# Performance work log

Hardware: AMD Instinct MI355X
Metric: run time of the kernel (lower is better)

## Reference

```python
import jax, jax.numpy as jnp
import numpy as np

N_HEADS = 16
HEAD_SIZE = 64

def setup_inputs() -> dict:
    key = jax.random.key(0)
    k1, k2 = jax.random.split(key)
    B, N, D = 2, 2048, N_HEADS * HEAD_SIZE
    x = jax.random.normal(k1, (B, N, D), dtype=jnp.float32)
    # lecun_normal-ish scale for the QKV kernel
    W_qkv = jax.random.normal(k2, (D, 3 * D), dtype=jnp.float32) * (1.0 / np.sqrt(D))
    return {"x": x, "W_qkv": W_qkv}

def reference(x, W_qkv):
    B, N, D = x.shape
    H, Dh = N_HEADS, HEAD_SIZE
    qkv = x @ W_qkv                                  # [B,N,3D]
    q, k, v = jnp.split(qkv, 3, axis=-1)
    q = q.reshape(B, N, H, Dh)
    k = k.reshape(B, N, H, Dh)
    v = v.reshape(B, N, H, Dh)
    dist = jnp.einsum('bihd,bjhd->bhij', q, k) / jnp.sqrt(jnp.asarray(Dh, dtype=x.dtype))
    mask = jnp.tril(jnp.ones((N, N), dtype=bool))[None, None, :, :]
    dist = jnp.where(mask, dist, -jnp.inf)
    attn = jax.nn.softmax(dist, axis=-1)             # [B,H,N,N]
    out_heads = jnp.einsum('bhij,bjhd->bihd', attn, v)
    return out_heads.reshape(B, N, H * Dh)
```

## Files before the change

### kernel.cpp

```cpp
#include <hip/hip_runtime.h>

typedef __attribute__((ext_vector_type(8))) short bf16x8;
typedef __attribute__((ext_vector_type(4))) float f32x4;
typedef __attribute__((ext_vector_type(16))) float f32x16;
typedef __attribute__((ext_vector_type(2))) unsigned int u32x2;

#define DEVI static __device__ __forceinline__

namespace {
constexpr int NSEQ = 2048, NH = 16;
constexpr int D = 1024, D3 = 3072;
}

DEVI unsigned short f2bf(float f) {
  union { float f; unsigned int u; } v; v.f = f;
  unsigned int r = v.u + 0x7FFFu + ((v.u >> 16) & 1u);
  return (unsigned short)(r >> 16);
}

DEVI void gload16(const unsigned short* g, unsigned short* lds_) {
  __builtin_amdgcn_global_load_lds(
      (const __attribute__((address_space(1))) unsigned int*)g,
      (__attribute__((address_space(3))) unsigned int*)lds_, 16, 0, 0);
}

DEVI f32x4 mfma16(bf16x8 a, bf16x8 b, f32x4 c) {
  return __builtin_amdgcn_mfma_f32_16x16x32_bf16(a, b, c, 0, 0, 0);
}

DEVI f32x16 mfma32(bf16x8 a, bf16x8 b, f32x16 c) {
  return __builtin_amdgcn_mfma_f32_32x32x16_bf16(a, b, c, 0, 0, 0);
}

DEVI float exp2g(float x) {
#if __has_builtin(__builtin_amdgcn_exp2f)
  return __builtin_amdgcn_exp2f(x);
#else
  return exp2f(x);
#endif
}

DEVI unsigned int cvtpk(float a, float b) {
  unsigned int r;
  asm("v_cvt_pk_bf16_f32 %0, %1, %2" : "=v"(r) : "v"(a), "v"(b));
  return r;
}

DEVI u32x2 pswap2(unsigned int a, unsigned int b) {
  return __builtin_amdgcn_permlane32_swap(a, b, false, false);
}
DEVI float xmax_halves(float v) {
  union { float f; unsigned int u; } c; c.f = v;
  u32x2 r = pswap2(c.u, c.u);
  union { unsigned int u; float f; } x, y; x.u = r.x; y.u = r.y;
  return fmaxf(x.f, y.f);
}

union U4 { unsigned int u[4]; bf16x8 v; };

__global__ __launch_bounds__(256) void prep_k(const float* __restrict__ x,
                                              const float* __restrict__ W,
                                              unsigned short* __restrict__ xb,
                                              unsigned short* __restrict__ Wt) {
  __shared__ float t[32][33];
  const int bid = blockIdx.x;
  if (bid < 4096) {
    int i = (bid * 256 + threadIdx.x) * 4;
    float4 v = *reinterpret_cast<const float4*>(x + i);
    ushort4 o;
    o.x = f2bf(v.x); o.y = f2bf(v.y); o.z = f2bf(v.z); o.w = f2bf(v.w);
    *reinterpret_cast<ushort4*>(xb + i) = o;
  } else {
    const int b2 = bid - 4096;
    const int c0 = (b2 % 96) * 32, k0 = (b2 / 96) * 32;
    const int tx = threadIdx.x & 31, ty = threadIdx.x >> 5;
#pragma unroll
    for (int r = 0; r < 32; r += 8)
      t[ty + r][tx] = W[(size_t)(k0 + ty + r) * D3 + c0 + tx];
    __syncthreads();
#pragma unroll
    for (int r = 0; r < 32; r += 8)
      Wt[(size_t)(c0 + ty + r) * D + k0 + tx] = f2bf(t[tx][ty + r]);
  }
}

__global__ __launch_bounds__(256) void qkv_gemm_k(const unsigned short* __restrict__ xb,
                                                  const unsigned short* __restrict__ Wt,
                                                  unsigned short* __restrict__ qw,
                                                  unsigned short* __restrict__ kw,
                                                  unsigned short* __restrict__ vtw) {
  __shared__ unsigned short smA[128 * 32];
  __shared__ unsigned short smB[128 * 32];
  const int tid = threadIdx.x, w = tid >> 6, l = tid & 63;
  const int m0 = blockIdx.x * 128, n0 = blockIdx.y * 128;
  const int wm = w >> 1, wn = w & 1;

  const unsigned short* ga[2]; const unsigned short* gb[2];
  unsigned short* la[2]; unsigned short* lb[2];
#pragma unroll
  for (int i = 0; i < 2; ++i) {
    int idx = tid + i * 256;
    int row = idx >> 2;
    int blk = (idx & 3) ^ ((row >> 1) & 3);
    ga[i] = xb + (size_t)(m0 + row) * D + blk * 8;
    gb[i] = Wt + (size_t)(n0 + row) * D + blk * 8;
    la[i] = smA + (w * 64 + i * 256) * 8;
    lb[i] = smB + (w * 64 + i * 256) * 8;
  }

  f32x4 acc[4][4];
#pragma unroll
  for (int a = 0; a < 4; ++a)
#pragma unroll
    for (int b = 0; b < 4; ++b) acc[a][b] = (f32x4){0.f, 0.f, 0.f, 0.f};

  for (int kt = 0; kt < D / 32; ++kt) {
    __syncthreads();
#pragma unroll
    for (int i = 0; i < 2; ++i) {
      gload16(ga[i] + kt * 32, la[i]);
      gload16(gb[i] + kt * 32, lb[i]);
    }
    asm volatile("s_waitcnt vmcnt(0)" ::: "memory");
    __syncthreads();

    bf16x8 af[4], bfr[4];
#pragma unroll
    for (int a = 0; a < 4; ++a) {
      int arow = wm * 64 + a * 16 + (l & 15);
      int blk = (l >> 4) ^ ((arow >> 1) & 3);
      af[a] = *reinterpret_cast<const bf16x8*>(smA + arow * 32 + blk * 8);
    }
#pragma unroll
    for (int b = 0; b < 4; ++b) {
      int brow = wn * 64 + b * 16 + (l & 15);
      int blk = (l >> 4) ^ ((brow >> 1) & 3);
      bfr[b] = *reinterpret_cast<const bf16x8*>(smB + brow * 32 + blk * 8);
    }
#pragma unroll
    for (int a = 0; a < 4; ++a)
#pragma unroll
      for (int b = 0; b < 4; ++b)
        acc[a][b] = mfma16(af[a], bfr[b], acc[a][b]);
  }

  const int which = n0 >> 10;
#pragma unroll
  for (int a = 0; a < 4; ++a) {
#pragma unroll
    for (int b = 0; b < 4; ++b) {
#pragma unroll
      for (int r = 0; r < 4; ++r) {
        int grow = m0 + wm * 64 + a * 16 + (l >> 4) * 4 + r;
        int gcol = n0 + wn * 64 + b * 16 + (l & 15);
        float v = acc[a][b][r];
        int bb = grow >> 11, n = grow & 2047;
        int cc = gcol & 1023, h = cc >> 6, dh = cc & 63;
        size_t bh = (size_t)bb * NH + h;
        if (which == 0)
          qw[(bh * NSEQ + n) * 64 + dh] = f2bf(v * 0.18033688011112042f);
        else if (which == 1)
          kw[(bh * NSEQ + n) * 64 + dh] = f2bf(v);
        else
          vtw[(bh * 64 + dh) * NSEQ + n] = f2bf(v);
      }
    }
  }
}

__global__ __launch_bounds__(256, 2) void attn_k(const unsigned short* __restrict__ qw,
                                                 const unsigned short* __restrict__ kw,
                                                 const unsigned short* __restrict__ vtw,
                                                 float* __restrict__ out) {
  __shared__ __align__(16) char lds[66560];
  const int tid = threadIdx.x, w = tid >> 6, l = tid & 63;
  const int hi = l >> 5, ql = l & 31;
  const int qsub = w >> 1, par = w & 1;

  const int wg = blockIdx.x;
  const int xcd = wg & 7, rest = wg >> 3;
  const int bhl = rest >> 4;
  const int j = rest & 15;
  const int bh = xcd * 4 + bhl;
  const int bb = bh >> 4, h = bh & 15;

  const unsigned short* qb = qw + (size_t)bh * NSEQ * 64;
  const unsigned short* kb = kw + (size_t)bh * NSEQ * 64;
  const unsigned short* vb = vtw + (size_t)bh * 64 * NSEQ;

  const int r0 = tid >> 3, c0 = (tid & 7) ^ (r0 & 7);
  const int r1 = (tid + 256) >> 3, c1 = ((tid + 256) & 7) ^ (r1 & 7);
  const int wbase = w * 512;

#define STAGE(SL, PR)                                                            \
  do {                                                                           \
    const int t0_ = 2 * (PR), t1_ = 2 * (PR) + 1;                                \
    unsigned short* k0d = (unsigned short*)(lds + (SL) * 32768) + wbase;         \
    unsigned short* v0d = (unsigned short*)(lds + (SL) * 32768 + 8192) + wbase;  \
    unsigned short* k1d = (unsigned short*)(lds + (SL) * 32768 + 16384) + wbase; \
    unsigned short* v1d = (unsigned short*)(lds + (SL) * 32768 + 24576) + wbase; \
    gload16(kb + (((size_t)t0_ * 64 + r0) * 64 + c0 * 8), k0d);                  \
    gload16(kb + (((size_t)t0_ * 64 + r1) * 64 + c1 * 8), k0d + 2048);           \
    gload16(vb + ((size_t)r0 * NSEQ + t0_ * 64 + c0 * 8), v0d);                  \
    gload16(vb + ((size_t)r1 * NSEQ + t0_ * 64 + c1 * 8), v0d + 2048);           \
    gload16(kb + (((size_t)t1_ * 64 + r0) * 64 + c0 * 8), k1d);                  \
    gload16(kb + (((size_t)t1_ * 64 + r1) * 64 + c1 * 8), k1d + 2048);           \
    gload16(vb + ((size_t)r0 * NSEQ + t1_ * 64 + c0 * 8), v1d);                  \
    gload16(vb + ((size_t)r1 * NSEQ + t1_ * 64 + c1 * 8), v1d + 2048);           \
  } while (0)

  for (int seg = 0; seg < 2; ++seg) {
    const int qt = seg ? j : (31 - j);
    const int qbase = qt * 64;
    const int qg = qbase + qsub * 32 + ql;

    bf16x8 qf[4];
#pragma unroll
    for (int ds = 0; ds < 4; ++ds)
      qf[ds] = *reinterpret_cast<const bf16x8*>(qb + (size_t)qg * 64 + ds * 16 + hi * 8);

    float m = -1e30f, lsum = 0.f;
    f32x16 O0, O1;
#pragma unroll
    for (int r2 = 0; r2 < 16; ++r2) { O0[r2] = 0.f; O1[r2] = 0.f; }

    const int nsup = (qt >> 1) + 1;
    STAGE(0, 0);
    for (int s = 0; s < nsup; ++s) {
      __syncthreads();
      if (s + 1 < nsup) STAGE((s + 1) & 1, s + 1);
      const int t = 2 * s + par;
      if (t <= qt) {
        const char* Kb = lds + (s & 1) * 32768 + par * 16384;
        const char* Vb = Kb + 8192;

        bf16x8 kf[8];
#pragma unroll
        for (int ds = 0; ds < 4; ++ds) {
          kf[ds] = *reinterpret_cast<const bf16x8*>(
              Kb + ql * 128 + (((2 * ds + hi) ^ (ql & 7)) << 4));
          kf[4 + ds] = *reinterpret_cast<const bf16x8*>(
              Kb + (32 + ql) * 128 + (((2 * ds + hi) ^ (ql & 7)) << 4));
        }

        f32x16 S0, S1;
#pragma unroll
        for (int r2 = 0; r2 < 16; ++r2) { S0[r2] = 0.f; S1[r2] = 0.f; }
        __builtin_amdgcn_s_setprio(1);
#pragma unroll
        for (int ds = 0; ds < 4; ++ds) {
          S0 = mfma32(kf[ds], qf[ds], S0);
          S1 = mfma32(kf[4 + ds], qf[ds], S1);
        }
        __builtin_amdgcn_s_setprio(0);

        bf16x8 vf[8];
#pragma unroll
        for (int ks = 0; ks < 4; ++ks) {
          vf[ks] = *reinterpret_cast<const bf16x8*>(
              Vb + ql * 128 + (((2 * ks + hi) ^ (ql & 7)) << 4));
          vf[4 + ks] = *reinterpret_cast<const bf16x8*>(
              Vb + (32 + ql) * 128 + (((2 * ks + hi) ^ (ql & 7)) << 4));
        }

        if (t == qt) {
#pragma unroll
          for (int reg = 0; reg < 16; ++reg) {
            const int krow = (reg & 3) + 8 * (reg >> 2) + 4 * hi;
            if (64 * t + krow > qg) S0[reg] = -1e30f;
            if (64 * t + 32 + krow > qg) S1[reg] = -1e30f;
          }
        }

        float t0 = fmaxf(S0[0], S1[0]), t1 = fmaxf(S0[1], S1[1]);
        float t2 = fmaxf(S0[2], S1[2]), t3 = fmaxf(S0[3], S1[3]);
#pragma unroll
        for (int r2 = 4; r2 < 16; r2 += 4) {
          t0 = fmaxf(t0, fmaxf(S0[r2], S1[r2]));
          t1 = fmaxf(t1, fmaxf(S0[r2 + 1], S1[r2 + 1]));
          t2 = fmaxf(t2, fmaxf(S0[r2 + 2], S1[r2 + 2]));
          t3 = fmaxf(t3, fmaxf(S0[r2 + 3], S1[r2 + 3]));
        }
        float tmax = xmax_halves(fmaxf(fmaxf(t0, t1), fmaxf(t2, t3)));

        if (!__all(tmax <= m + 8.0f)) {
          const float mn = fmaxf(m, tmax);
          const float g = exp2g(m - mn);
          m = mn;
          lsum *= g;
#pragma unroll
          for (int r2 = 0; r2 < 16; ++r2) { O0[r2] *= g; O1[r2] *= g; }
        }

        float pr0[16], pr1[16];
        float rA = 0.f, rB = 0.f, rC = 0.f, rD = 0.f;
#pragma unroll
        for (int r2 = 0; r2 < 16; r2 += 4) {
          pr0[r2] = exp2g(S0[r2] - m);     pr1[r2] = exp2g(S1[r2] - m);
          pr0[r2 + 1] = exp2g(S0[r2 + 1] - m); pr1[r2 + 1] = exp2g(S1[r2 + 1] - m);
          pr0[r2 + 2] = exp2g(S0[r2 + 2] - m); pr1[r2 + 2] = exp2g(S1[r2 + 2] - m);
          pr0[r2 + 3] = exp2g(S0[r2 + 3] - m); pr1[r2 + 3] = exp2g(S1[r2 + 3] - m);
          rA += pr0[r2] + pr1[r2];
          rB += pr0[r2 + 1] + pr1[r2 + 1];
          rC += pr0[r2 + 2] + pr1[r2 + 2];
          rD += pr0[r2 + 3] + pr1[r2 + 3];
        }
        {
          float rsum = (rA + rB) + (rC + rD);
          union { float f; unsigned int u; } c; c.f = rsum;
          u32x2 r = pswap2(c.u, c.u);
          union { unsigned int u; float f; } x, y; x.u = r.x; y.u = r.y;
          lsum += x.f + y.f;
        }

        bf16x8 pf[4];
#pragma unroll
        for (int ct = 0; ct < 2; ++ct) {
          const float* pp = ct ? pr1 : pr0;
          unsigned int u[4][2];
#pragma unroll
          for (int c = 0; c < 4; ++c) {
            u[c][0] = cvtpk(pp[4 * c], pp[4 * c + 1]);
            u[c][1] = cvtpk(pp[4 * c + 2], pp[4 * c + 3]);
          }
#pragma unroll
          for (int kk = 0; kk < 2; ++kk) {
            u32x2 rw0 = pswap2(u[2 * kk][0], u[2 * kk + 1][0]);
            u32x2 rw1 = pswap2(u[2 * kk][1], u[2 * kk + 1][1]);
            U4 f;
            f.u[0] = rw0.x; f.u[1] = rw1.x;
            f.u[2] = rw0.y; f.u[3] = rw1.y;
            pf[2 * ct + kk] = f.v;
          }
        }

        __builtin_amdgcn_s_setprio(1);
#pragma unroll
        for (int ks = 0; ks < 4; ++ks) {
          O0 = mfma32(vf[ks], pf[ks], O0);
          O1 = mfma32(vf[4 + ks], pf[ks], O1);
        }
        __builtin_amdgcn_s_setprio(0);
      }
    }

    __syncthreads();
    float* mlp = (float*)(lds + 65536);
    if (l < 32) { mlp[w * 64 + l] = m; mlp[w * 64 + 32 + l] = lsum; }
    __syncthreads();
    {
      const int pw = w ^ 1;
      const float m1 = mlp[pw * 64 + ql];
      const float l1 = mlp[pw * 64 + 32 + ql];
      const float M = fmaxf(m, m1);
      const float g0 = exp2g(m - M);
      const float g1 = exp2g(m1 - M);
      const float L = lsum * g0 + l1 * g1;
      const float phi = g0 / L;
      float* mo = (float*)lds + (qsub * 2 + par) * 2048;
#pragma unroll
      for (int reg = 0; reg < 16; ++reg) {
        const int dr = (reg & 3) + 8 * (reg >> 2) + 4 * hi;
        const int d1 = 32 + dr;
        mo[ql * 64 + (((dr >> 2) ^ (ql & 7)) << 2) + (dr & 3)] = O0[reg] * phi;
        mo[ql * 64 + (((d1 >> 2) ^ (ql & 7)) << 2) + (d1 & 3)] = O1[reg] * phi;
      }
    }
    __syncthreads();
    {
      const int qq = tid >> 2, dq = (tid & 3) << 4;
      const float* pa = (float*)lds + ((qq >> 5) * 2 + 0) * 2048 + (qq & 31) * 64;
      const float* pb = (float*)lds + ((qq >> 5) * 2 + 1) * 2048 + (qq & 31) * 64;
      float* op = out + ((size_t)bb * NSEQ + qbase + qq) * D + h * 64 + dq;
#pragma unroll
      for (int c = 0; c < 4; ++c) {
        const int ch = ((dq >> 2) + c) ^ (qq & 7);
        float4 va = *reinterpret_cast<const float4*>(pa + ch * 4);
        float4 vb4 = *reinterpret_cast<const float4*>(pb + ch * 4);
        float4 s4 = make_float4(va.x + vb4.x, va.y + vb4.y, va.z + vb4.z, va.w + vb4.w);
        *reinterpret_cast<float4*>(op + c * 4) = s4;
      }
    }
    __syncthreads();
  }
#undef STAGE
}

extern "C" void kernel_launch(void* const* d_in, const int* in_sizes, int n_in,
                              void* d_out, int out_size, void* d_ws, size_t ws_size,
                              hipStream_t stream) {
  const float* x = (const float*)d_in[0];
  const float* W = (const float*)d_in[1];
  float* out = (float*)d_out;
  char* ws = (char*)d_ws;
  unsigned short* xb  = (unsigned short*)(ws);
  unsigned short* Wt  = (unsigned short*)(ws + 8388608);
  unsigned short* qw  = (unsigned short*)(ws + 14680064);
  unsigned short* kw  = (unsigned short*)(ws + 23068672);
  unsigned short* vtw = (unsigned short*)(ws + 31457280);

  prep_k<<<7168, 256, 0, stream>>>(x, W, xb, Wt);
  qkv_gemm_k<<<dim3(32, 24), 256, 0, stream>>>(xb, Wt, qw, kw, vtw);
  attn_k<<<512, 256, 0, stream>>>(qw, kw, vtw, out);
}
```

Baseline: 84.09 us.

## Fuse the two causal query tiles into a single KV sweep sharing K/V loads

Each block previously ran the paired high and low query tiles one after the other, streaming K/V from global into LDS separately for each. The new code keeps both tiles' Q fragments, softmax state and accumulators live together and sweeps K/V once over the longer range. For early KV tiles it also computes the low tile's scores and PV. This removes the duplicate K/V staging, LDS fragment reads and barriers for the low tile. The cost is roughly double the accumulator registers (four f32x16 outputs plus two score tiles), which may lower occupancy or cause spills.

```diff
diff --git a/kernel.cpp b/kernel.cpp
--- a/kernel.cpp
+++ b/kernel.cpp
@@ -54,6 +54,12 @@
   u32x2 r = pswap2(c.u, c.u);
   union { unsigned int u; float f; } x, y; x.u = r.x; y.u = r.y;
   return fmaxf(x.f, y.f);
+}
+DEVI float xsum_halves(float v) {
+  union { float f; unsigned int u; } c; c.f = v;
+  u32x2 r = pswap2(c.u, c.u);
+  union { unsigned int u; float f; } x, y; x.u = r.x; y.u = r.y;
+  return x.f + y.f;
 }
 
 union U4 { unsigned int u[4]; bf16x8 v; };
@@ -209,181 +215,194 @@
     gload16(vb + ((size_t)r1 * NSEQ + t1_ * 64 + c1 * 8), v1d + 2048);           \
   } while (0)
 
-  for (int seg = 0; seg < 2; ++seg) {
-    const int qt = seg ? j : (31 - j);
-    const int qbase = qt * 64;
-    const int qg = qbase + qsub * 32 + ql;
-
-    bf16x8 qf[4];
-#pragma unroll
-    for (int ds = 0; ds < 4; ++ds)
-      qf[ds] = *reinterpret_cast<const bf16x8*>(qb + (size_t)qg * 64 + ds * 16 + hi * 8);
-
-    float m = -1e30f, lsum = 0.f;
-    f32x16 O0, O1;
-#pragma unroll
-    for (int r2 = 0; r2 < 16; ++r2) { O0[r2] = 0.f; O1[r2] = 0.f; }
-
-    const int nsup = (qt >> 1) + 1;
-    STAGE(0, 0);
-    for (int s = 0; s < nsup; ++s) {
-      __syncthreads();
-      if (s + 1 < nsup) STAGE((s + 1) & 1, s + 1);
-      const int t = 2 * s + par;
-      if (t <= qt) {
-        const char* Kb = lds + (s & 1) * 32768 + par * 16384;
-        const char* Vb = Kb + 8192;
-
-        bf16x8 kf[8];
+#define TILE_SM_PV(T, QT, QG, M, LSUM, S0, S1, O0v, O1v, VF)                     \
+  do {                                                                           \
+    if ((T) == (QT)) {                                                           \
+      _Pragma("unroll") for (int reg = 0; reg < 16; ++reg) {                     \
+        const int krow = (reg & 3) + 8 * (reg >> 2) + 4 * hi;                    \
+        if (64 * (T) + krow > (QG)) S0[reg] = -1e30f;                            \
+        if (64 * (T) + 32 + krow > (QG)) S1[reg] = -1e30f;                       \
+      }                                                                          \
+    }                                                                            \
+    float t0 = fmaxf(S0[0], S1[0]), t1 = fmaxf(S0[1], S1[1]);                    \
+    float t2 = fmaxf(S0[2], S1[2]), t3 = fmaxf(S0[3], S1[3]);                    \
+    _Pragma("unroll") for (int r2 = 4; r2 < 16; r2 += 4) {                       \
+      t0 = fmaxf(t0, fmaxf(S0[r2], S1[r2]));                                     \
+      t1 = fmaxf(t1, fmaxf(S0[r2 + 1], S1[r2 + 1]));                             \
+      t2 = fmaxf(t2, fmaxf(S0[r2 + 2], S1[r2 + 2]));                             \
+      t3 = fmaxf(t3, fmaxf(S0[r2 + 3], S1[r2 + 3]));                             \
+    }                                                                            \
+    float tmax = xmax_halves(fmaxf(fmaxf(t0, t1), fmaxf(t2, t3)));               \
+    if (!__all(tmax <= (M) + 8.0f)) {                                            \
+      const float mn = fmaxf((M), tmax);                                         \
+      const float g = exp2g((M)-mn);                                             \
+      (M) = mn;                                                                  \
+      (LSUM) *= g;                                                               \
+      _Pragma("unroll") for (int r2 = 0; r2 < 16; ++r2) {                        \
+        O0v[r2] *= g; O1v[r2] *= g;                                              \
+      }                                                                          \
+    }                                                                            \
+    float rA = 0.f, rB = 0.f, rC = 0.f, rD = 0.f;                                \
+    _Pragma("unroll") for (int r2 = 0; r2 < 16; r2 += 4) {                       \
+      S0[r2] = exp2g(S0[r2] - (M));         S1[r2] = exp2g(S1[r2] - (M));        \
+      S0[r2 + 1] = exp2g(S0[r2 + 1] - (M)); S1[r2 + 1] = exp2g(S1[r2 + 1] - (M));\
+      S0[r2 + 2] = exp2g(S0[r2 + 2] - (M)); S1[r2 + 2] = exp2g(S1[r2 + 2] - (M));\
+      S0[r2 + 3] = exp2g(S0[r2 + 3] - (M)); S1[r2 + 3] = exp2g(S1[r2 + 3] - (M));\
+      rA += S0[r2] + S1[r2];                                                     \
+      rB += S0[r2 + 1] + S1[r2 + 1];                                             \
+      rC += S0[r2 + 2] + S1[r2 + 2];                                             \
+      rD += S0[r2 + 3] + S1[r2 + 3];                                             \
+    }                                                                            \
+    (LSUM) += xsum_halves((rA + rB) + (rC + rD));                                \
+    bf16x8 pf[4];                                                                \
+    _Pragma("unroll") for (int ct = 0; ct < 2; ++ct) {                           \
+      unsigned int u[4][2];                                                      \
+      _Pragma("unroll") for (int c = 0; c < 4; ++c) {                            \
+        if (ct == 0) {                                                           \
+          u[c][0] = cvtpk(S0[4 * c], S0[4 * c + 1]);                             \
+          u[c][1] = cvtpk(S0[4 * c + 2], S0[4 * c + 3]);                         \
+        } else {                                                                 \
+          u[c][0] = cvtpk(S1[4 * c], S1[4 * c + 1]);                             \
+          u[c][1] = cvtpk(S1[4 * c + 2], S1[4 * c + 3]);                         \
+        }                                                                        \
+      }                                                                          \
+      _Pragma("unroll") for (int kk = 0; kk < 2; ++kk) {                         \
+        u32x2 rw0 = pswap2(u[2 * kk][0], u[2 * kk + 1][0]);                      \
+        u32x2 rw1 = pswap2(u[2 * kk][1], u[2 * kk + 1][1]);                      \
+        U4 f;                                                                    \
+        f.u[0] = rw0.x; f.u[1] = rw1.x;                                          \
+        f.u[2] = rw0.y; f.u[3] = rw1.y;                                          \
+        pf[2 * ct + kk] = f.v;                                                   \
+      }                                                                          \
+    }                                                                            \
+    __builtin_amdgcn_s_setprio(1);                                               \
+    _Pragma("unroll") for (int ks = 0; ks < 4; ++ks) {                           \
+      O0v = mfma32(VF[ks], pf[ks], O0v);                                         \
+      O1v = mfma32(VF[4 + ks], pf[ks], O1v);                                     \
+    }                                                                            \
+    __builtin_amdgcn_s_setprio(0);                                               \
+  } while (0)
+
+#define EPILOGUE(M, LSUM, O0v, O1v, QBASE)                                       \
+  do {                                                                           \
+    __syncthreads();                                                             \
+    float* mlp = (float*)(lds + 65536);                                          \
+    if (l < 32) { mlp[w * 64 + l] = (M); mlp[w * 64 + 32 + l] = (LSUM); }        \
+    __syncthreads();                                                             \
+    {                                                                            \
+      const int pw = w ^ 1;                                                      \
+      const float m1 = mlp[pw * 64 + ql];                                        \
+      const float l1 = mlp[pw * 64 + 32 + ql];                                   \
+      const float M_ = fmaxf((M), m1);                                           \
+      const float g0 = exp2g((M)-M_);                                            \
+      const float g1 = exp2g(m1 - M_);                                           \
+      const float L = (LSUM)*g0 + l1 * g1;                                       \
+      const float phi = g0 / L;                                                  \
+      float* mo = (float*)lds + (qsub * 2 + par) * 2048;                         \
+      _Pragma("unroll") for (int reg = 0; reg < 16; ++reg) {                     \
+        const int dr = (reg & 3) + 8 * (reg >> 2) + 4 * hi;                      \
+        const int d1 = 32 + dr;                                                  \
+        mo[ql * 64 + (((dr >> 2) ^ (ql & 7)) << 2) + (dr & 3)] = O0v[reg] * phi; \
+        mo[ql * 64 + (((d1 >> 2) ^ (ql & 7)) << 2) + (d1 & 3)] = O1v[reg] * phi; \
+      }                                                                          \
+    }                                                                            \
+    __syncthreads();                                                             \
+    {                                                                            \
+      const int qq = tid >> 2, dq = (tid & 3) << 4;                              \
+      const float* pa = (float*)lds + ((qq >> 5) * 2 + 0) * 2048 + (qq & 31) * 64;\
+      const float* pb = (float*)lds + ((qq >> 5) * 2 + 1) * 2048 + (qq & 31) * 64;\
+      float* op = out + ((size_t)bb * NSEQ + (QBASE) + qq) * D + h * 64 + dq;    \
+      _Pragma("unroll") for (int c = 0; c < 4; ++c) {                            \
+        const int ch = ((dq >> 2) + c) ^ (qq & 7);                               \
+        float4 va = *reinterpret_cast<const float4*>(pa + ch * 4);               \
+        float4 vb4 = *reinterpret_cast<const float4*>(pb + ch * 4);              \
+        float4 s4 = make_float4(va.x + vb4.x, va.y + vb4.y, va.z + vb4.z,        \
+                                va.w + vb4.w);                                   \
+        *reinterpret_cast<float4*>(op + c * 4) = s4;                             \
+      }                                                                          \
+    }                                                                            \
+  } while (0)
+
+  const int qtH = 31 - j, qtL = j;
+  const int qgH = qtH * 64 + qsub * 32 + ql;
+  const int qgL = qtL * 64 + qsub * 32 + ql;
+
+  bf16x8 qfH[4], qfL[4];
+#pragma unroll
+  for (int ds = 0; ds < 4; ++ds) {
+    qfH[ds] = *reinterpret_cast<const bf16x8*>(qb + (size_t)qgH * 64 + ds * 16 + hi * 8);
+    qfL[ds] = *reinterpret_cast<const bf16x8*>(qb + (size_t)qgL * 64 + ds * 16 + hi * 8);
+  }
+
+  float mH = -1e30f, lsumH = 0.f, mL = -1e30f, lsumL = 0.f;
+  f32x16 OH0, OH1, OL0, OL1;
+#pragma unroll
+  for (int r2 = 0; r2 < 16; ++r2) {
+    OH0[r2] = 0.f; OH1[r2] = 0.f; OL0[r2] = 0.f; OL1[r2] = 0.f;
+  }
+
+  const int nsup = (qtH >> 1) + 1;
+  STAGE(0, 0);
+  for (int s = 0; s < nsup; ++s) {
+    __syncthreads();
+    if (s + 1 < nsup) STAGE((s + 1) & 1, s + 1);
+    const int t = 2 * s + par;
+    if (t <= qtH) {
+      const char* Kb = lds + (s & 1) * 32768 + par * 16384;
+      const char* Vb = Kb + 8192;
+      const bool liveL = (t <= qtL);
+
+      bf16x8 kf[8];
+#pragma unroll
+      for (int ds = 0; ds < 4; ++ds) {
+        kf[ds] = *reinterpret_cast<const bf16x8*>(
+            Kb + ql * 128 + (((2 * ds + hi) ^ (ql & 7)) << 4));
+        kf[4 + ds] = *reinterpret_cast<const bf16x8*>(
+            Kb + (32 + ql) * 128 + (((2 * ds + hi) ^ (ql & 7)) << 4));
+      }
+
+      f32x16 SH0, SH1, SL0, SL1;
+#pragma unroll
+      for (int r2 = 0; r2 < 16; ++r2) { SH0[r2] = 0.f; SH1[r2] = 0.f; }
+      __builtin_amdgcn_s_setprio(1);
+#pragma unroll
+      for (int ds = 0; ds < 4; ++ds) {
+        SH0 = mfma32(kf[ds], qfH[ds], SH0);
+        SH1 = mfma32(kf[4 + ds], qfH[ds], SH1);
+      }
+      if (liveL) {
+#pragma unroll
+        for (int r2 = 0; r2 < 16; ++r2) { SL0[r2] = 0.f; SL1[r2] = 0.f; }
 #pragma unroll
         for (int ds = 0; ds < 4; ++ds) {
-          kf[ds] = *reinterpret_cast<const bf16x8*>(
-              Kb + ql * 128 + (((2 * ds + hi) ^ (ql & 7)) << 4));
-          kf[4 + ds] = *reinterpret_cast<const bf16x8*>(
-              Kb + (32 + ql) * 128 + (((2 * ds + hi) ^ (ql & 7)) << 4));
+          SL0 = mfma32(kf[ds], qfL[ds], SL0);
+          SL1 = mfma32(kf[4 + ds], qfL[ds], SL1);
         }
-
-        f32x16 S0, S1;
-#pragma unroll
-        for (int r2 = 0; r2 < 16; ++r2) { S0[r2] = 0.f; S1[r2] = 0.f; }
-        __builtin_amdgcn_s_setprio(1);
-#pragma unroll
-        for (int ds = 0; ds < 4; ++ds) {
-          S0 = mfma32(kf[ds], qf[ds], S0);
-          S1 = mfma32(kf[4 + ds], qf[ds], S1);
-        }
-        __builtin_amdgcn_s_setprio(0);
-
-        bf16x8 vf[8];
-#pragma unroll
-        for (int ks = 0; ks < 4; ++ks) {
-          vf[ks] = *reinterpret_cast<const bf16x8*>(
-              Vb + ql * 128 + (((2 * ks + hi) ^ (ql & 7)) << 4));
-          vf[4 + ks] = *reinterpret_cast<const bf16x8*>(
-              Vb + (32 + ql) * 128 + (((2 * ks + hi) ^ (ql & 7)) << 4));
-        }
-
-        if (t == qt) {
-#pragma unroll
-          for (int reg = 0; reg < 16; ++reg) {
-            const int krow = (reg & 3) + 8 * (reg >> 2) + 4 * hi;
-            if (64 * t + krow > qg) S0[reg] = -1e30f;
-            if (64 * t + 32 + krow > qg) S1[reg] = -1e30f;
-          }
-        }
-
-        float t0 = fmaxf(S0[0], S1[0]), t1 = fmaxf(S0[1], S1[1]);
-        float t2 = fmaxf(S0[2], S1[2]), t3 = fmaxf(S0[3], S1[3]);
-#pragma unroll
-        for (int r2 = 4; r2 < 16; r2 += 4) {
-          t0 = fmaxf(t0, fmaxf(S0[r2], S1[r2]));
-          t1 = fmaxf(t1, fmaxf(S0[r2 + 1], S1[r2 + 1]));
-          t2 = fmaxf(t2, fmaxf(S0[r2 + 2], S1[r2 + 2]));
-          t3 = fmaxf(t3, fmaxf(S0[r2 + 3], S1[r2 + 3]));
-        }
-        float tmax = xmax_halves(fmaxf(fmaxf(t0, t1), fmaxf(t2, t3)));
-
-        if (!__all(tmax <= m + 8.0f)) {
-          const float mn = fmaxf(m, tmax);
-          const float g = exp2g(m - mn);
-          m = mn;
-          lsum *= g;
-#pragma unroll
-          for (int r2 = 0; r2 < 16; ++r2) { O0[r2] *= g; O1[r2] *= g; }
-        }
-
-        float pr0[16], pr1[16];
-        float rA = 0.f, rB = 0.f, rC = 0.f, rD = 0.f;
-#pragma unroll
-        for (int r2 = 0; r2 < 16; r2 += 4) {
-          pr0[r2] = exp2g(S0[r2] - m);     pr1[r2] = exp2g(S1[r2] - m);
-          pr0[r2 + 1] = exp2g(S0[r2 + 1] - m); pr1[r2 + 1] = exp2g(S1[r2 + 1] - m);
-          pr0[r2 + 2] = exp2g(S0[r2 + 2] - m); pr1[r2 + 2] = exp2g(S1[r2 + 2] - m);
-          pr0[r2 + 3] = exp2g(S0[r2 + 3] - m); pr1[r2 + 3] = exp2g(S1[r2 + 3] - m);
-          rA += pr0[r2] + pr1[r2];
-          rB += pr0[r2 + 1] + pr1[r2 + 1];
-          rC += pr0[r2 + 2] + pr1[r2 + 2];
-          rD += pr0[r2 + 3] + pr1[r2 + 3];
-        }
-        {
-          float rsum = (rA + rB) + (rC + rD);
-          union { float f; unsigned int u; } c; c.f = rsum;
-          u32x2 r = pswap2(c.u, c.u);
-          union { unsigned int u; float f; } x, y; x.u = r.x; y.u = r.y;
-          lsum += x.f + y.f;
-        }
-
-        bf16x8 pf[4];
-#pragma unroll
-        for (int ct = 0; ct < 2; ++ct) {
-          const float* pp = ct ? pr1 : pr0;
-          unsigned int u[4][2];
-#pragma unroll
-          for (int c = 0; c < 4; ++c) {
-            u[c][0] = cvtpk(pp[4 * c], pp[4 * c + 1]);
-            u[c][1] = cvtpk(pp[4 * c + 2], pp[4 * c + 3]);
-          }
-#pragma unroll
-          for (int kk = 0; kk < 2; ++kk) {
-            u32x2 rw0 = pswap2(u[2 * kk][0], u[2 * kk + 1][0]);
-            u32x2 rw1 = pswap2(u[2 * kk][1], u[2 * kk + 1][1]);
-            U4 f;
-            f.u[0] = rw0.x; f.u[1] = rw1.x;
-            f.u[2] = rw0.y; f.u[3] = rw1.y;
-            pf[2 * ct + kk] = f.v;
-          }
-        }
-
-        __builtin_amdgcn_s_setprio(1);
-#pragma unroll
-        for (int ks = 0; ks < 4; ++ks) {
-          O0 = mfma32(vf[ks], pf[ks], O0);
-          O1 = mfma32(vf[4 + ks], pf[ks], O1);
-        }
-        __builtin_amdgcn_s_setprio(0);
+      }
+      __builtin_amdgcn_s_setprio(0);
+
+      bf16x8 vf[8];
+#pragma unroll
+      for (int ks = 0; ks < 4; ++ks) {
+        vf[ks] = *reinterpret_cast<const bf16x8*>(
+            Vb + ql * 128 + (((2 * ks + hi) ^ (ql & 7)) << 4));
+        vf[4 + ks] = *reinterpret_cast<const bf16x8*>(
+            Vb + (32 + ql) * 128 + (((2 * ks + hi) ^ (ql & 7)) << 4));
+      }
+
+      TILE_SM_PV(t, qtH, qgH, mH, lsumH, SH0, SH1, OH0, OH1, vf);
+      if (liveL) {
+        TILE_SM_PV(t, qtL, qgL, mL, lsumL, SL0, SL1, OL0, OL1, vf);
       }
     }
-
-    __syncthreads();
-    float* mlp = (float*)(lds + 65536);
-    if (l < 32) { mlp[w * 64 + l] = m; mlp[w * 64 + 32 + l] = lsum; }
-    __syncthreads();
-    {
-      const int pw = w ^ 1;
-      const float m1 = mlp[pw * 64 + ql];
-      const float l1 = mlp[pw * 64 + 32 + ql];
-      const float M = fmaxf(m, m1);
-      const float g0 = exp2g(m - M);
-      const float g1 = exp2g(m1 - M);
-      const float L = lsum * g0 + l1 * g1;
-      const float phi = g0 / L;
-      float* mo = (float*)lds + (qsub * 2 + par) * 2048;
-#pragma unroll
-      for (int reg = 0; reg < 16; ++reg) {
-        const int dr = (reg & 3) + 8 * (reg >> 2) + 4 * hi;
-        const int d1 = 32 + dr;
-        mo[ql * 64 + (((dr >> 2) ^ (ql & 7)) << 2) + (dr & 3)] = O0[reg] * phi;
-        mo[ql * 64 + (((d1 >> 2) ^ (ql & 7)) << 2) + (d1 & 3)] = O1[reg] * phi;
-      }
-    }
-    __syncthreads();
-    {
-      const int qq = tid >> 2, dq = (tid & 3) << 4;
-      const float* pa = (float*)lds + ((qq >> 5) * 2 + 0) * 2048 + (qq & 31) * 64;
-      const float* pb = (float*)lds + ((qq >> 5) * 2 + 1) * 2048 + (qq & 31) * 64;
-      float* op = out + ((size_t)bb * NSEQ + qbase + qq) * D + h * 64 + dq;
-#pragma unroll
-      for (int c = 0; c < 4; ++c) {
-        const int ch = ((dq >> 2) + c) ^ (qq & 7);
-        float4 va = *reinterpret_cast<const float4*>(pa + ch * 4);
-        float4 vb4 = *reinterpret_cast<const float4*>(pb + ch * 4);
-        float4 s4 = make_float4(va.x + vb4.x, va.y + vb4.y, va.z + vb4.z, va.w + vb4.w);
-        *reinterpret_cast<float4*>(op + c * 4) = s4;
-      }
-    }
-    __syncthreads();
-  }
+  }
+
+  EPILOGUE(mH, lsumH, OH0, OH1, qtH * 64);
+  __syncthreads();
+  EPILOGUE(mL, lsumL, OL0, OL1, qtL * 64);
 #undef STAGE
+#undef TILE_SM_PV
+#undef EPILOGUE
 }
 
 extern "C" void kernel_launch(void* const* d_in, const int* in_sizes, int n_in,
```

Measured after the change: 84.29 us. No clear change (+0.2%).
